# Optimization experiments

Hardware: AMD Instinct MI355X
Metric: run time of the kernel (lower is better)

Reference implementation:

```python
import jax, jax.numpy as jnp
import numpy as np

B, S, D = 4, 2048, 1024
H = 16
HD = D // H

def setup_inputs() -> dict:
    key = jax.random.key(0)
    ks = jax.random.split(key, 6)
    std = 1.0 / np.sqrt(D)
    x = jax.random.normal(ks[0], (B, S, D), dtype=jnp.float32)
    Wq = jax.random.uniform(ks[1], (D, D), jnp.float32, -std, std)
    Wk = jax.random.uniform(ks[2], (D, D), jnp.float32, -std, std)
    Wv = jax.random.uniform(ks[3], (D, D), jnp.float32, -std, std)
    Wo = jax.random.uniform(ks[4], (D, D), jnp.float32, -std, std)
    bo = jax.random.uniform(ks[5], (D,), jnp.float32, -std, std)
    return {"x": x, "Wq": Wq, "Wk": Wk, "Wv": Wv, "Wo": Wo, "bo": bo}

def reference(x, Wq, Wk, Wv, Wo, bo):
    b, s, _ = x.shape
    # projections; torch Linear computes x @ W^T, here W stored as (d_in, d_out)... we use (D, D) applied as x @ W
    q = (x @ Wq).reshape(b, s, H, HD).transpose(0, 2, 1, 3)  # b h s hd
    k = (x @ Wk).reshape(b, s, H, HD).transpose(0, 2, 1, 3)
    v = (x @ Wv).reshape(b, s, H, HD).transpose(0, 2, 1, 3)
    scores = jnp.einsum('bhqd,bhkd->bhqk', q, k)
    causal = jnp.triu(jnp.ones((s, s), dtype=bool), k=1)
    scores = jnp.where(causal[None, None], -jnp.inf, scores)
    attn = jax.nn.softmax(scores / np.sqrt(HD), axis=-1)  # dropout=0.0 -> identity
    ctx = jnp.einsum('bhqk,bhkd->bhqd', attn, v)
    ctx = ctx.transpose(0, 2, 1, 3).reshape(b, s, D)
    return ctx @ Wo + bo
```

## Files before the change

kernel.cpp:

```cpp
#include <hip/hip_runtime.h>

typedef unsigned short u16;
typedef __bf16 bf16x8 __attribute__((ext_vector_type(8)));
typedef float f32x4 __attribute__((ext_vector_type(4)));

#define Bn 4
#define Sn 2048
#define Dn 1024
#define Hn 16
#define HDn 64

__device__ inline u16 f2bf(float f) {
  unsigned u = __builtin_bit_cast(unsigned, f);
  u += 0x7fffu + ((u >> 16) & 1u);
  return (u16)(u >> 16);
}

__device__ __forceinline__ void gl2lds16(const u16* g, u16* l) {
  __builtin_amdgcn_global_load_lds(
      (const __attribute__((address_space(1))) unsigned int*)g,
      (__attribute__((address_space(3))) unsigned int*)l, 16, 0, 0);
}

__device__ __forceinline__ float fexp2(float x) {
  return __builtin_amdgcn_exp2f(x);
}

__device__ __forceinline__ unsigned pk_bf_trunc(float lo, float hi) {
  return __builtin_amdgcn_perm(__builtin_bit_cast(unsigned, hi),
                               __builtin_bit_cast(unsigned, lo), 0x07060302u);
}

__global__ __launch_bounds__(256) void cvt4(const float* __restrict__ in,
                                            u16* __restrict__ out, int n4) {
  int i = blockIdx.x * 256 + threadIdx.x;
  if (i < n4) {
    float4 v = ((const float4*)in)[i];
    ushort4 o;
    o.x = f2bf(v.x); o.y = f2bf(v.y); o.z = f2bf(v.z); o.w = f2bf(v.w);
    ((ushort4*)out)[i] = o;
  }
}

__global__ __launch_bounds__(256) void tcvt4(const float* __restrict__ w0,
                                             const float* __restrict__ w1,
                                             const float* __restrict__ w2,
                                             const float* __restrict__ w3,
                                             u16* __restrict__ out) {
  __shared__ u16 tile[32][33];
  const float* in = (blockIdx.z == 0) ? w0 : (blockIdx.z == 1) ? w1
                   : (blockIdx.z == 2) ? w2 : w3;
  u16* dst = out + (size_t)blockIdx.z * Dn * Dn;
  int bx = blockIdx.x * 32;
  int by = blockIdx.y * 32;
  int tx = threadIdx.x & 31;
  int ty = threadIdx.x >> 5;
#pragma unroll
  for (int r = 0; r < 32; r += 8)
    tile[ty + r][tx] = f2bf(in[(size_t)(by + ty + r) * Dn + bx + tx]);
  __syncthreads();
#pragma unroll
  for (int r = 0; r < 32; r += 8)
    dst[(size_t)(bx + ty + r) * Dn + by + tx] = tile[tx][ty + r];
}

#define MFMA16(a, b, c) __builtin_amdgcn_mfma_f32_16x16x32_bf16(a, b, c, 0, 0, 0)

#define SRCP_INIT(APTR, BPTR)                                                \
  const u16* srcp[3][2];                                                     \
  _Pragma("unroll") for (int rg = 0; rg < 3; rg++) {                         \
    _Pragma("unroll") for (int j = 0; j < 2; j++) {                          \
      int o = j * 8192 + tid * 16;                                           \
      int l = o ^ (((o >> 8) & 7) << 4);                                     \
      int rho = l >> 7;                                                      \
      int c2 = (l >> 1) & 63;                                                \
      int gr;                                                                \
      if (rg == 0)      gr = bm + rho;                                       \
      else if (rg == 1) gr = bn + ((rho >> 5) << 6) + (rho & 31);            \
      else              gr = bn + ((rho >> 5) << 6) + 32 + (rho & 31);       \
      const u16* base = (rg == 0) ? (APTR) : (BPTR);                         \
      srcp[rg][j] = base + (size_t)gr * Dn + c2;                             \
    }                                                                        \
  }

#define ARD(D, Q, F, K)                                                      \
  (*(const bf16x8*)((const char*)&S[D][0][0] +                               \
      ((wr * 64 + (Q) * 32 + (F) * 16 + lcol) * 128 + ((K) ? cs1 : cs0))))
#define BRD(D, NI, K)                                                        \
  (*(const bf16x8*)((const char*)&S[D][1 + ((NI) >> 1)][0] +                 \
      ((wc * 32 + ((NI) & 1) * 16 + lcol) * 128 + ((K) ? cs1 : cs0))))

#define VM6 asm volatile("s_waitcnt vmcnt(6)" ::: "memory")
#define VM0 asm volatile("s_waitcnt vmcnt(0)" ::: "memory")

#define KTILE(D, DN, T, WAIT)                                                \
  {                                                                          \
    stg(0, DN, (T) + 2); stg(1, DN, (T) + 2); stg(2, DN, (T) + 2);           \
    bf16x8 a00 = ARD(D, 0, 0, 0), a01 = ARD(D, 0, 0, 1);                     \
    bf16x8 a10 = ARD(D, 0, 1, 0), a11 = ARD(D, 0, 1, 1);                     \
    bf16x8 a20 = ARD(D, 1, 0, 0), a21 = ARD(D, 1, 0, 1);                     \
    bf16x8 a30 = ARD(D, 1, 1, 0), a31 = ARD(D, 1, 1, 1);                     \
    bf16x8 bk0[4], bk1[4];                                                   \
    _Pragma("unroll") for (int ni = 0; ni < 4; ni++) {                       \
      bk0[ni] = BRD(D, ni, 0); bk1[ni] = BRD(D, ni, 1);                      \
    }                                                                        \
    asm volatile("s_waitcnt lgkmcnt(0)" ::: "memory");                       \
    __builtin_amdgcn_sched_barrier(0);                                       \
    __builtin_amdgcn_s_setprio(1);                                           \
    _Pragma("unroll") for (int ni = 0; ni < 4; ni++) {                       \
      acc[0][ni] = MFMA16(a00, bk0[ni], acc[0][ni]);                         \
      acc[1][ni] = MFMA16(a10, bk0[ni], acc[1][ni]);                         \
      acc[2][ni] = MFMA16(a20, bk0[ni], acc[2][ni]);                         \
      acc[3][ni] = MFMA16(a30, bk0[ni], acc[3][ni]);                         \
    }                                                                        \
    _Pragma("unroll") for (int ni = 0; ni < 4; ni++) {                       \
      acc[0][ni] = MFMA16(a01, bk1[ni], acc[0][ni]);                         \
      acc[1][ni] = MFMA16(a11, bk1[ni], acc[1][ni]);                         \
      acc[2][ni] = MFMA16(a21, bk1[ni], acc[2][ni]);                         \
      acc[3][ni] = MFMA16(a31, bk1[ni], acc[3][ni]);                         \
    }                                                                        \
    __builtin_amdgcn_s_setprio(0);                                           \
    WAIT;                                                                    \
    __builtin_amdgcn_s_barrier();                                            \
    __builtin_amdgcn_sched_barrier(0);                                       \
  }

#define KLOOP                                                                \
  stg(0, 0, 0); stg(1, 0, 0); stg(2, 0, 0);                                  \
  stg(0, 1, 1); stg(1, 1, 1); stg(2, 1, 1);                                  \
  VM6;                                                                       \
  __builtin_amdgcn_s_barrier();                                              \
  __builtin_amdgcn_sched_barrier(0);                                         \
  _Pragma("unroll 1") for (int I = 0; I < 5; ++I) {                          \
    const int T0 = 3 * I;                                                    \
    KTILE(0, 2, T0, VM6)                                                     \
    KTILE(1, 0, T0 + 1, VM6)                                                 \
    KTILE(2, 1, T0 + 2, if (I == 4) { VM0; } else { VM6; })                  \
  }                                                                          \
  KTILE(0, 2, 15, )

__global__ __launch_bounds__(512, 2) void gemm_qkv(const u16* __restrict__ A,
                                                   const u16* __restrict__ Bt,
                                                   u16* __restrict__ qkb,
                                                   u16* __restrict__ vt,
                                                   float qscale) {
  __shared__ __attribute__((aligned(16))) u16 S[3][3][8192];

  const int tid = threadIdx.x;
  const int lane = tid & 63;
  const int lcol = lane & 15;
  const int quad = lane >> 4;
  const int wave = tid >> 6;
  const int wr = wave >> 2;
  const int wc = wave & 3;

  const int bid = blockIdx.x;
  const int idx = bid >> 3;
  const int bm = (((bid & 7) << 3) + (idx & 7)) * 128;
  const int bn = (idx >> 3) * 256;

  SRCP_INIT(A, Bt)

  auto stg = [&](int rg, int buf, int tile) {
    if (tile >= 16) return;
    const int k0 = tile << 6;
    u16* d = &S[buf][rg][tid * 8];
    gl2lds16(srcp[rg][0] + k0, d);
    gl2lds16(srcp[rg][1] + k0, d + 4096);
  };

  f32x4 acc[4][4];
#pragma unroll
  for (int i = 0; i < 4; i++)
#pragma unroll
    for (int j = 0; j < 4; j++) acc[i][j] = (f32x4){0.f, 0.f, 0.f, 0.f};

  const int SW = (lcol & 14) << 3;
  const int cs0 = (quad * 16) ^ SW;
  const int cs1 = (64 + quad * 16) ^ SW;

  KLOOP

  const int rb = bm + wr * 64 + quad * 4;
  const int cb = bn + wc * 64 + lcol;
  if (bn >= 2048) {
#pragma unroll
    for (int mi = 0; mi < 4; mi++) {
#pragma unroll
      for (int ni = 0; ni < 4; ni++) {
        int row0 = rb + mi * 16;
        int s = row0 & (Sn - 1);
        int bb = row0 >> 11;
        int vcol = cb + ni * 16 - 2048;
        int bh = (bb << 4) + (vcol >> 6);
        int hd = vcol & 63;
        unsigned d0 = (unsigned)f2bf(acc[mi][ni][0]) |
                      ((unsigned)f2bf(acc[mi][ni][1]) << 16);
        unsigned d1 = (unsigned)f2bf(acc[mi][ni][2]) |
                      ((unsigned)f2bf(acc[mi][ni][3]) << 16);
        *(uint2*)(vt + ((size_t)bh * HDn + hd) * Sn + s) = (uint2){d0, d1};
      }
    }
  } else {
    const float scale = (bn < 1024) ? qscale : 1.0f;
#pragma unroll
    for (int mi = 0; mi < 4; mi++) {
#pragma unroll
      for (int ni = 0; ni < 4; ni++) {
        int row0 = rb + mi * 16;
        int col = cb + ni * 16;
#pragma unroll
        for (int r = 0; r < 4; r++)
          qkb[(size_t)(row0 + r) * 2048 + col] = f2bf(acc[mi][ni][r] * scale);
      }
    }
  }
}

__global__ __launch_bounds__(512, 2) void gemm_out(const u16* __restrict__ A,
                                                   const u16* __restrict__ Bt,
                                                   float* __restrict__ Cout,
                                                   const float* __restrict__ bias) {
  __shared__ __attribute__((aligned(16))) u16 S[3][3][8192];

  const int tid = threadIdx.x;
  const int lane = tid & 63;
  const int lcol = lane & 15;
  const int quad = lane >> 4;
  const int wave = tid >> 6;
  const int wr = wave >> 2;
  const int wc = wave & 3;

  const int bid = blockIdx.x;
  const int idx = bid >> 3;
  const int bm = (((bid & 7) << 3) + (idx & 7)) * 128;
  const int bn = (idx >> 3) * 256;

  SRCP_INIT(A, Bt)

  auto stg = [&](int rg, int buf, int tile) {
    if (tile >= 16) return;
    const int k0 = tile << 6;
    u16* d = &S[buf][rg][tid * 8];
    gl2lds16(srcp[rg][0] + k0, d);
    gl2lds16(srcp[rg][1] + k0, d + 4096);
  };

  f32x4 acc[4][4];
#pragma unroll
  for (int i = 0; i < 4; i++)
#pragma unroll
    for (int j = 0; j < 4; j++) acc[i][j] = (f32x4){0.f, 0.f, 0.f, 0.f};

  const int SW = (lcol & 14) << 3;
  const int cs0 = (quad * 16) ^ SW;
  const int cs1 = (64 + quad * 16) ^ SW;

  KLOOP

  const int rb = bm + wr * 64 + quad * 4;
  const int cb = bn + wc * 64 + lcol;
  float bv[4];
#pragma unroll
  for (int ni = 0; ni < 4; ni++) bv[ni] = bias[cb + ni * 16];
#pragma unroll
  for (int mi = 0; mi < 4; mi++) {
#pragma unroll
    for (int ni = 0; ni < 4; ni++) {
      int row0 = rb + mi * 16;
      int col = cb + ni * 16;
#pragma unroll
      for (int r = 0; r < 4; r++)
        Cout[(size_t)(row0 + r) * Dn + col] = acc[mi][ni][r] + bv[ni];
    }
  }
}

__global__ __launch_bounds__(256, 2) void attn5(const u16* __restrict__ QK,
                                                const u16* __restrict__ Vt,
                                                u16* __restrict__ ctx) {
  __shared__ __attribute__((aligned(16))) u16 Ks2[2][64][32];
  __shared__ __attribute__((aligned(16))) u16 Vts2[2][64][32];
  __shared__ __attribute__((aligned(16))) u16 Pt[4][32][72];

  const int bh = blockIdx.x;
  const int b = bh >> 4, h = bh & 15;
  const int pair = blockIdx.y;
  const int t = threadIdx.x;
  const int w = t >> 6;
  const int lane = t & 63;
  const int lcol = lane & 15;
  const int quad = lane >> 4;
  const int qw0 = pair * 128 + w * 32;
  const int qw1 = (15 - pair) * 128 + w * 32;

  const size_t qkbase = ((size_t)b * Sn) * 2048 + h * HDn;
  const size_t obase = ((size_t)b * Sn) * Dn + h * HDn;
  const size_t vbase = ((size_t)bh * HDn) * Sn;

  bf16x8 qf[2][2][2];
#pragma unroll
  for (int si = 0; si < 2; si++) {
    const int qws = si ? qw1 : qw0;
#pragma unroll
    for (int qb = 0; qb < 2; qb++) {
      const u16* qp = QK + qkbase + (size_t)(qws + qb * 16 + lcol) * 2048 + quad * 8;
      qf[si][qb][0] = *(const bf16x8*)qp;
      qf[si][qb][1] = *(const bf16x8*)(qp + 32);
    }
  }

  f32x4 o[2][2][4];
#pragma unroll
  for (int si = 0; si < 2; si++)
#pragma unroll
    for (int qb = 0; qb < 2; qb++)
#pragma unroll
      for (int nb = 0; nb < 4; nb++) o[si][qb][nb] = (f32x4){0.f, 0.f, 0.f, 0.f};
  float lsum[2][2] = {{0.f, 0.f}, {0.f, 0.f}};

  const int srow = lane >> 2;
  const int sseg = (lane & 3) * 8;
  const u16* kp0 = QK + qkbase + 1024 + (size_t)(w * 16 + srow) * 2048 + sseg;
  const u16* vp0 = Vt + vbase + (size_t)(w * 16 + srow) * Sn + sseg;
  u16* ksl0 = &Ks2[0][0][0] + w * 512 + lane * 8;
  u16* ksl1 = ksl0 + 2048;
  u16* vsl0 = &Vts2[0][0][0] + w * 512 + lane * 8;
  u16* vsl1 = vsl0 + 2048;

  auto do_strip = [&](int si, int qw, int j0) {
    f32x4 s[4][2];
#pragma unroll
    for (int mb = 0; mb < 4; mb++) {
      bf16x8 kf0 = *(const bf16x8*)(&Ks2[0][mb * 16 + lcol][quad * 8]);
      bf16x8 kf1 = *(const bf16x8*)(&Ks2[1][mb * 16 + lcol][quad * 8]);
#pragma unroll
      for (int qb = 0; qb < 2; qb++) {
        f32x4 a = (f32x4){0.f, 0.f, 0.f, 0.f};
        a = __builtin_amdgcn_mfma_f32_16x16x32_bf16(kf0, qf[si][qb][0], a, 0, 0, 0);
        a = __builtin_amdgcn_mfma_f32_16x16x32_bf16(kf1, qf[si][qb][1], a, 0, 0, 0);
        s[mb][qb] = a;
      }
    }

    const bool needmask = (j0 + 63 > qw);
#pragma unroll
    for (int qb = 0; qb < 2; qb++) {
      const int qrow = qw + qb * 16 + lcol;
#pragma unroll
      for (int mb = 0; mb < 4; mb++) {
        float p[4];
#pragma unroll
        for (int r = 0; r < 4; r++) p[r] = fexp2(s[mb][qb][r]);
        if (needmask) {
          const int kvb = j0 + mb * 16 + quad * 4;
#pragma unroll
          for (int r = 0; r < 4; r++)
            if (kvb + r > qrow) p[r] = 0.f;
        }
        lsum[si][qb] += (p[0] + p[1]) + (p[2] + p[3]);
        unsigned d0 = pk_bf_trunc(p[0], p[1]);
        unsigned d1 = pk_bf_trunc(p[2], p[3]);
        *(uint2*)(&Pt[w][qb * 16 + lcol][mb * 16 + quad * 4]) = (uint2){d0, d1};
      }
    }

#pragma unroll
    for (int c = 0; c < 2; c++) {
      bf16x8 pf0 = *(const bf16x8*)(&Pt[w][lcol][c * 32 + quad * 8]);
      bf16x8 pf1 = *(const bf16x8*)(&Pt[w][16 + lcol][c * 32 + quad * 8]);
#pragma unroll
      for (int nb = 0; nb < 4; nb++) {
        bf16x8 vf = *(const bf16x8*)(&Vts2[c][nb * 16 + lcol][quad * 8]);
        o[si][0][nb] = __builtin_amdgcn_mfma_f32_16x16x32_bf16(vf, pf0, o[si][0][nb], 0, 0, 0);
        o[si][1][nb] = __builtin_amdgcn_mfma_f32_16x16x32_bf16(vf, pf1, o[si][1][nb], 0, 0, 0);
      }
    }
  };

  const int n_kv = (15 - pair) * 128 + 128;

  for (int j0 = 0; j0 < n_kv; j0 += 64) {
    {
      const u16* kp = kp0 + (size_t)j0 * 2048;
      gl2lds16(kp, ksl0);
      gl2lds16(kp + 32, ksl1);
      const u16* vp = vp0 + j0;
      gl2lds16(vp, vsl0);
      gl2lds16(vp + 32, vsl1);
    }
    __syncthreads();

    if (j0 <= qw1 + 31) do_strip(1, qw1, j0);
    if (j0 <= qw0 + 31) do_strip(0, qw0, j0);
    __syncthreads();
  }

#pragma unroll
  for (int si = 0; si < 2; si++) {
    const int qws = si ? qw1 : qw0;
#pragma unroll
    for (int qb = 0; qb < 2; qb++) {
      float l = lsum[si][qb];
      l += __shfl_xor(l, 16);
      l += __shfl_xor(l, 32);
      float inv = 1.0f / l;
#pragma unroll
      for (int nb = 0; nb < 4; nb++) {
        unsigned d0 = (unsigned)f2bf(o[si][qb][nb][0] * inv) |
                      ((unsigned)f2bf(o[si][qb][nb][1] * inv) << 16);
        unsigned d1 = (unsigned)f2bf(o[si][qb][nb][2] * inv) |
                      ((unsigned)f2bf(o[si][qb][nb][3] * inv) << 16);
        u16* p = ctx + obase + (size_t)(qws + qb * 16 + lcol) * Dn + nb * 16 + quad * 4;
        *(uint2*)p = (uint2){d0, d1};
      }
    }
  }
}

extern "C" void kernel_launch(void* const* d_in, const int* in_sizes, int n_in,
                              void* d_out, int out_size, void* d_ws, size_t ws_size,
                              hipStream_t stream) {
  const float* x  = (const float*)d_in[0];
  const float* Wq = (const float*)d_in[1];
  const float* Wk = (const float*)d_in[2];
  const float* Wv = (const float*)d_in[3];
  const float* Wo = (const float*)d_in[4];
  const float* bo = (const float*)d_in[5];
  float* out = (float*)d_out;

  const size_t BSD = (size_t)Bn * Sn * Dn;
  const size_t DD = (size_t)Dn * Dn;

  u16* xb    = (u16*)d_ws;
  u16* wall  = xb + BSD;
  u16* qkb   = wall + 4 * DD;
  u16* vt    = qkb + 2 * BSD;
  u16* cb    = vt + BSD;

  cvt4<<<(int)(BSD / 4 / 256), 256, 0, stream>>>(x, xb, (int)(BSD / 4));
  tcvt4<<<dim3(Dn / 32, Dn / 32, 4), 256, 0, stream>>>(Wq, Wk, Wv, Wo, wall);

  gemm_qkv<<<dim3(768), 512, 0, stream>>>(xb, wall, qkb, vt,
                                          0.125f * 1.44269504f);

  attn5<<<dim3(Bn * Hn, 8), 256, 0, stream>>>(qkb, vt, cb);

  gemm_out<<<dim3(256), 512, 0, stream>>>(cb, wall + 3 * DD, out, bo);
}
```

Before: 225.3 us.

## Double-buffer K/V tiles in attention and split LDS fragment reads in GEMM

The attention kernel now keeps two LDS buffers for K and V tiles and issues the async global-to-LDS load for the next tile before computing on the current one. It waits with vmcnt(4), so loads overlap compute instead of sitting behind a full sync every iteration. The GEMM K-tile macro drops the blanket lgkmcnt(0) wait and reorders its fragment loads so the first half of the MFMAs can start before the second half arrives. The cost is double the K/V LDS footprint and reliance on hand-placed wait counts and barriers being correct.

Result: slower. 238.4 us (+5.8%).

```diff
diff --git a/kernel.cpp b/kernel.cpp
--- a/kernel.cpp
+++ b/kernel.cpp
@@ -96,16 +96,14 @@
 #define KTILE(D, DN, T, WAIT)                                                \
   {                                                                          \
     stg(0, DN, (T) + 2); stg(1, DN, (T) + 2); stg(2, DN, (T) + 2);           \
-    bf16x8 a00 = ARD(D, 0, 0, 0), a01 = ARD(D, 0, 0, 1);                     \
-    bf16x8 a10 = ARD(D, 0, 1, 0), a11 = ARD(D, 0, 1, 1);                     \
-    bf16x8 a20 = ARD(D, 1, 0, 0), a21 = ARD(D, 1, 0, 1);                     \
-    bf16x8 a30 = ARD(D, 1, 1, 0), a31 = ARD(D, 1, 1, 1);                     \
+    __builtin_amdgcn_sched_barrier(0);                                       \
+    bf16x8 a00 = ARD(D, 0, 0, 0), a10 = ARD(D, 0, 1, 0);                     \
+    bf16x8 a20 = ARD(D, 1, 0, 0), a30 = ARD(D, 1, 1, 0);                     \
     bf16x8 bk0[4], bk1[4];                                                   \
-    _Pragma("unroll") for (int ni = 0; ni < 4; ni++) {                       \
-      bk0[ni] = BRD(D, ni, 0); bk1[ni] = BRD(D, ni, 1);                      \
-    }                                                                        \
-    asm volatile("s_waitcnt lgkmcnt(0)" ::: "memory");                       \
-    __builtin_amdgcn_sched_barrier(0);                                       \
+    _Pragma("unroll") for (int ni = 0; ni < 4; ni++) bk0[ni] = BRD(D, ni, 0);\
+    bf16x8 a01 = ARD(D, 0, 0, 1), a11 = ARD(D, 0, 1, 1);                     \
+    bf16x8 a21 = ARD(D, 1, 0, 1), a31 = ARD(D, 1, 1, 1);                     \
+    _Pragma("unroll") for (int ni = 0; ni < 4; ni++) bk1[ni] = BRD(D, ni, 1);\
     __builtin_amdgcn_s_setprio(1);                                           \
     _Pragma("unroll") for (int ni = 0; ni < 4; ni++) {                       \
       acc[0][ni] = MFMA16(a00, bk0[ni], acc[0][ni]);                         \
@@ -279,8 +277,8 @@
 __global__ __launch_bounds__(256, 2) void attn5(const u16* __restrict__ QK,
                                                 const u16* __restrict__ Vt,
                                                 u16* __restrict__ ctx) {
-  __shared__ __attribute__((aligned(16))) u16 Ks2[2][64][32];
-  __shared__ __attribute__((aligned(16))) u16 Vts2[2][64][32];
+  __shared__ __attribute__((aligned(16))) u16 Ks2[2][2][64][32];
+  __shared__ __attribute__((aligned(16))) u16 Vts2[2][2][64][32];
   __shared__ __attribute__((aligned(16))) u16 Pt[4][32][72];
 
   const int bh = blockIdx.x;
@@ -323,17 +321,26 @@
   const int sseg = (lane & 3) * 8;
   const u16* kp0 = QK + qkbase + 1024 + (size_t)(w * 16 + srow) * 2048 + sseg;
   const u16* vp0 = Vt + vbase + (size_t)(w * 16 + srow) * Sn + sseg;
-  u16* ksl0 = &Ks2[0][0][0] + w * 512 + lane * 8;
-  u16* ksl1 = ksl0 + 2048;
-  u16* vsl0 = &Vts2[0][0][0] + w * 512 + lane * 8;
-  u16* vsl1 = vsl0 + 2048;
-
-  auto do_strip = [&](int si, int qw, int j0) {
+  u16* ksl = &Ks2[0][0][0][0] + w * 512 + lane * 8;
+  u16* vsl = &Vts2[0][0][0][0] + w * 512 + lane * 8;
+
+  auto stg_kv = [&](int bs, int j0) {
+    const u16* kp = kp0 + (size_t)j0 * 2048;
+    const u16* vp = vp0 + j0;
+    u16* kd = ksl + bs * 4096;
+    u16* vd = vsl + bs * 4096;
+    gl2lds16(kp, kd);
+    gl2lds16(kp + 32, kd + 2048);
+    gl2lds16(vp, vd);
+    gl2lds16(vp + 32, vd + 2048);
+  };
+
+  auto do_strip = [&](int si, int qw, int j0, int bs) {
     f32x4 s[4][2];
 #pragma unroll
     for (int mb = 0; mb < 4; mb++) {
-      bf16x8 kf0 = *(const bf16x8*)(&Ks2[0][mb * 16 + lcol][quad * 8]);
-      bf16x8 kf1 = *(const bf16x8*)(&Ks2[1][mb * 16 + lcol][quad * 8]);
+      bf16x8 kf0 = *(const bf16x8*)(&Ks2[bs][0][mb * 16 + lcol][quad * 8]);
+      bf16x8 kf1 = *(const bf16x8*)(&Ks2[bs][1][mb * 16 + lcol][quad * 8]);
 #pragma unroll
       for (int qb = 0; qb < 2; qb++) {
         f32x4 a = (f32x4){0.f, 0.f, 0.f, 0.f};
@@ -371,7 +378,7 @@
       bf16x8 pf1 = *(const bf16x8*)(&Pt[w][16 + lcol][c * 32 + quad * 8]);
 #pragma unroll
       for (int nb = 0; nb < 4; nb++) {
-        bf16x8 vf = *(const bf16x8*)(&Vts2[c][nb * 16 + lcol][quad * 8]);
+        bf16x8 vf = *(const bf16x8*)(&Vts2[bs][c][nb * 16 + lcol][quad * 8]);
         o[si][0][nb] = __builtin_amdgcn_mfma_f32_16x16x32_bf16(vf, pf0, o[si][0][nb], 0, 0, 0);
         o[si][1][nb] = __builtin_amdgcn_mfma_f32_16x16x32_bf16(vf, pf1, o[si][1][nb], 0, 0, 0);
       }
@@ -379,21 +386,27 @@
   };
 
   const int n_kv = (15 - pair) * 128 + 128;
-
-  for (int j0 = 0; j0 < n_kv; j0 += 64) {
-    {
-      const u16* kp = kp0 + (size_t)j0 * 2048;
-      gl2lds16(kp, ksl0);
-      gl2lds16(kp + 32, ksl1);
-      const u16* vp = vp0 + j0;
-      gl2lds16(vp, vsl0);
-      gl2lds16(vp + 32, vsl1);
-    }
-    __syncthreads();
-
-    if (j0 <= qw1 + 31) do_strip(1, qw1, j0);
-    if (j0 <= qw0 + 31) do_strip(0, qw0, j0);
-    __syncthreads();
+  const int nit = n_kv >> 6;
+
+  stg_kv(0, 0);
+#pragma unroll 1
+  for (int it = 0; it < nit; ++it) {
+    const int j0 = it << 6;
+    const int bs = it & 1;
+    if (it + 1 < nit) {
+      stg_kv(bs ^ 1, j0 + 64);
+      asm volatile("s_waitcnt vmcnt(4)" ::: "memory");
+    } else {
+      asm volatile("s_waitcnt vmcnt(0)" ::: "memory");
+    }
+    __builtin_amdgcn_s_barrier();
+    __builtin_amdgcn_sched_barrier(0);
+
+    if (j0 <= qw1 + 31) do_strip(1, qw1, j0, bs);
+    if (j0 <= qw0 + 31) do_strip(0, qw0, j0, bs);
+
+    __builtin_amdgcn_s_barrier();
+    __builtin_amdgcn_sched_barrier(0);
   }
 
 #pragma unroll
```
